# Performance work log

Hardware: AMD Instinct MI355X
Metric: run time of the kernel (lower is better)

## Reference

```python
import jax, jax.numpy as jnp
import numpy as np

B, H, N, M = 8192, 512, 1024, 128
EPS_COS = 1e-8   # torch cosine_similarity default eps
EPS_NORM = 1e-16 # normalization eps in forward


def _linear_params(key, fan_in, fan_out):
    # torch nn.Linear default init: U(-1/sqrt(fan_in), 1/sqrt(fan_in))
    lim = 1.0 / np.sqrt(fan_in)
    kw, kb = jax.random.split(key)
    W = jax.random.uniform(kw, (fan_out, fan_in), minval=-lim, maxval=lim, dtype=jnp.float32)
    b = jax.random.uniform(kb, (fan_out,), minval=-lim, maxval=lim, dtype=jnp.float32)
    return W, b


def setup_inputs() -> dict:
    key = jax.random.key(0)
    ks = jax.random.split(key, 8)
    Wk, bk = _linear_params(ks[0], H, M)
    Wb, bb = _linear_params(ks[1], H, 1)
    Wg, bg = _linear_params(ks[2], H, 1)
    Ws, bs = _linear_params(ks[3], H, N)
    Wgam, bgam = _linear_params(ks[4], H, 1)
    x = jax.random.normal(ks[5], (B, H), dtype=jnp.float32)
    # previous_state is an attention-weight vector over memory rows (sums to 1)
    previous_state = jax.nn.softmax(jax.random.normal(ks[6], (B, N), dtype=jnp.float32), axis=-1)
    memory = jax.random.normal(ks[7], (N, M), dtype=jnp.float32)
    return dict(x=x, previous_state=previous_state, memory=memory,
                Wk=Wk, bk=bk, Wb=Wb, bb=bb, Wg=Wg, bg=bg,
                Ws=Ws, bs=bs, Wgam=Wgam, bgam=bgam)


def _circular_convolution(w, s):
    # Full circular convolution over the memory axis:
    #   out[b, i] = sum_j w[b, j] * s[b, (i - j) mod N]
    # Implemented via FFT to avoid materializing a [B, N, N] shift matrix.
    out = jnp.fft.irfft(jnp.fft.rfft(w, axis=-1) * jnp.fft.rfft(s, axis=-1),
                        n=w.shape[-1], axis=-1)
    # conv of nonnegative weights is nonnegative; clamp tiny FFT round-off
    # negatives so the fractional power below stays well defined.
    return jnp.maximum(out, 0.0)


def reference(x, previous_state, memory, Wk, bk, Wb, bb, Wg, bg, Ws, bs, Wgam, bgam):
    k = x @ Wk.T + bk                                   # [B, M]
    beta = jax.nn.softplus(x @ Wb.T + bb)               # [B, 1]
    g = jax.nn.sigmoid(x @ Wg.T + bg)                   # [B, 1]
    s = jax.nn.softmax(x @ Ws.T + bs, axis=-1)          # [B, N]
    gamma = 1.0 + jax.nn.softplus(x @ Wgam.T + bgam)    # [B, 1]

    # cosine similarity between each key and each memory row -> [B, N]
    k_n = k / jnp.maximum(jnp.linalg.norm(k, axis=-1, keepdims=True), EPS_COS)
    m_n = memory / jnp.maximum(jnp.linalg.norm(memory, axis=-1, keepdims=True), EPS_COS)
    cos = k_n @ m_n.T                                   # [B, N]

    w_c = jax.nn.softmax(beta * cos, axis=1)            # content addressing
    w_g = g * w_c + (1.0 - g) * previous_state          # interpolation gate
    w_t = _circular_convolution(w_g, s)                 # location shift
    w = w_t ** gamma                                    # sharpening
    w = w / (jnp.sum(w, axis=1, keepdims=True) + EPS_NORM)

    read = w @ memory                                   # [B, M]
    return read, w
```

## Files before the change

kernel.cpp:

```cpp
#include <hip/hip_runtime.h>
#include <hip/hip_bf16.h>
#include <hip/hip_fp16.h>

typedef __attribute__((ext_vector_type(8))) short short8;
typedef __attribute__((ext_vector_type(4))) short short4v;
typedef __attribute__((ext_vector_type(4))) float f32x4;

#define B_ROWS 8192
#define HDIM 512
#define NDIM 1024
#define MDIM 128

__device__ __forceinline__ float softplusf(float z) {
  return fmaxf(z, 0.f) + log1pf(__expf(-fabsf(z)));
}
__device__ __forceinline__ unsigned short f2bfu(float f) {
  __hip_bfloat16 h = __float2bfloat16(f);
  return *reinterpret_cast<unsigned short*>(&h);
}
__device__ __forceinline__ short8 pack8(float4 a, float4 b) {
  short8 r;
  r[0] = (short)f2bfu(a.x); r[1] = (short)f2bfu(a.y);
  r[2] = (short)f2bfu(a.z); r[3] = (short)f2bfu(a.w);
  r[4] = (short)f2bfu(b.x); r[5] = (short)f2bfu(b.y);
  r[6] = (short)f2bfu(b.z); r[7] = (short)f2bfu(b.w);
  return r;
}
__device__ __forceinline__ int pad(int i) { return i + (i >> 4); }

__global__ __launch_bounds__(256) void prep_all(
    const float* __restrict__ x, const float* __restrict__ Ws,
    const float* __restrict__ Wk, const float* __restrict__ mem,
    const float* __restrict__ Wb, const float* __restrict__ bb,
    const float* __restrict__ Wg, const float* __restrict__ bg,
    const float* __restrict__ Wgam, const float* __restrict__ bgam,
    short* __restrict__ xb, short* __restrict__ wsb, short* __restrict__ wkb,
    short* __restrict__ mn_bf, short* __restrict__ memT_bf,
    float* __restrict__ bgg)
{
  const int blk = blockIdx.x, t = threadIdx.x;
  if (blk < 512) {
    __shared__ float sredp[4];
    const int half = t >> 7, tl = t & 127;
    const int n = blk * 2 + half;
    const int wid = t >> 6;
    const float v = mem[n * MDIM + tl];
    float ss = v * v;
#pragma unroll
    for (int o = 32; o; o >>= 1) ss += __shfl_xor(ss, o);
    if ((t & 63) == 0) sredp[wid] = ss;
    __syncthreads();
    const float inv = 1.f / fmaxf(sqrtf(sredp[half * 2] + sredp[half * 2 + 1]), 1e-8f);
    mn_bf[n * MDIM + tl] = (short)f2bfu(v * inv);
    memT_bf[(size_t)tl * NDIM + n] = (short)f2bfu(v);
  } else if (blk < 2560) {
    const int wid = t >> 6, lane = t & 63;
    const int b = (blk - 512) * 4 + wid;
    const size_t xo = (size_t)b * HDIM + lane * 8;
    const float4 x0 = *(const float4*)(x + xo);
    const float4 x1 = *(const float4*)(x + xo + 4);
    *(short8*)(xb + xo) = pack8(x0, x1);
    const float4 b0 = *(const float4*)(Wb + lane * 8);
    const float4 b1 = *(const float4*)(Wb + lane * 8 + 4);
    const float4 g0 = *(const float4*)(Wg + lane * 8);
    const float4 g1 = *(const float4*)(Wg + lane * 8 + 4);
    const float4 m0 = *(const float4*)(Wgam + lane * 8);
    const float4 m1 = *(const float4*)(Wgam + lane * 8 + 4);
    float zb = x0.x*b0.x + x0.y*b0.y + x0.z*b0.z + x0.w*b0.w
             + x1.x*b1.x + x1.y*b1.y + x1.z*b1.z + x1.w*b1.w;
    float zg = x0.x*g0.x + x0.y*g0.y + x0.z*g0.z + x0.w*g0.w
             + x1.x*g1.x + x1.y*g1.y + x1.z*g1.z + x1.w*g1.w;
    float zm = x0.x*m0.x + x0.y*m0.y + x0.z*m0.z + x0.w*m0.w
             + x1.x*m1.x + x1.y*m1.y + x1.z*m1.z + x1.w*m1.w;
#pragma unroll
    for (int o = 32; o; o >>= 1) {
      zb += __shfl_xor(zb, o); zg += __shfl_xor(zg, o); zm += __shfl_xor(zm, o);
    }
    if (lane == 0) {
      zb += bb[0]; zg += bg[0]; zm += bgam[0];
      bgg[b * 4 + 0] = softplusf(zb);
      bgg[b * 4 + 1] = 1.f / (1.f + __expf(-zg));
      bgg[b * 4 + 2] = 1.f + softplusf(zm);
    }
  } else {
    const int NS4 = NDIM * HDIM / 4;
    const int NK4 = MDIM * HDIM / 4;
    const int stride = 144 * 256;
    for (int i = (blk - 2560) * 256 + t; i < NS4 + NK4; i += stride) {
      const float* src; short* dst; int j = i;
      if (j < NS4) { src = Ws; dst = wsb; }
      else { j -= NS4; src = Wk; dst = wkb; }
      const float4 v = ((const float4*)src)[j];
      short4v o;
      o[0] = (short)f2bfu(v.x); o[1] = (short)f2bfu(v.y);
      o[2] = (short)f2bfu(v.z); o[3] = (short)f2bfu(v.w);
      ((short4v*)dst)[j] = o;
    }
  }
}

__global__ __launch_bounds__(256) void kgemm_norm(
    const short* __restrict__ xb, const short* __restrict__ wkb,
    const float* __restrict__ bk, short* __restrict__ khat)
{
  __shared__ __align__(16) short sA[32][40];
  __shared__ __align__(16) short sW[128][40];
  __shared__ float snorm[4][32];
  __shared__ float sinv[32];

  const int tid = threadIdx.x, lane = tid & 63, wid = tid >> 6;
  const int bm = blockIdx.x;
  const int fr = lane & 15, kg = (lane >> 4) << 3;

  f32x4 acc[2][2] = {};

  for (int k0 = 0; k0 < HDIM; k0 += 32) {
    if (k0) __syncthreads();
    if (tid < 128) {
      const int row = tid >> 2, c0 = (tid & 3) * 8;
      *(short8*)(&sA[row][c0]) =
          *(const short8*)(xb + (size_t)(bm * 32 + row) * HDIM + k0 + c0);
    }
#pragma unroll
    for (int u = tid; u < 512; u += 256) {
      const int row = u >> 2, c0 = (u & 3) * 8;
      *(short8*)(&sW[row][c0]) =
          *(const short8*)(wkb + (size_t)row * HDIM + k0 + c0);
    }
    __syncthreads();

    short8 af[2], bf[2];
#pragma unroll
    for (int i = 0; i < 2; i++) af[i] = *(const short8*)(&sA[i * 16 + fr][kg]);
#pragma unroll
    for (int n = 0; n < 2; n++) bf[n] = *(const short8*)(&sW[wid * 32 + n * 16 + fr][kg]);
#pragma unroll
    for (int i = 0; i < 2; i++)
#pragma unroll
      for (int n = 0; n < 2; n++)
        acc[i][n] = __builtin_amdgcn_mfma_f32_16x16x32_bf16(af[i], bf[n], acc[i][n], 0, 0, 0);
  }

  const int rbase = (lane >> 4) << 2;
  float z[2][2][4];
#pragma unroll
  for (int i = 0; i < 2; i++)
#pragma unroll
    for (int n = 0; n < 2; n++) {
      const float bv = bk[wid * 32 + n * 16 + fr];
#pragma unroll
      for (int r = 0; r < 4; r++) z[i][n][r] = acc[i][n][r] + bv;
    }
#pragma unroll
  for (int i = 0; i < 2; i++)
#pragma unroll
    for (int r = 0; r < 4; r++) {
      float sq = z[i][0][r] * z[i][0][r] + z[i][1][r] * z[i][1][r];
      sq += __shfl_xor(sq, 1); sq += __shfl_xor(sq, 2);
      sq += __shfl_xor(sq, 4); sq += __shfl_xor(sq, 8);
      if (fr == 0) snorm[wid][i * 16 + rbase + r] = sq;
    }
  __syncthreads();
  if (tid < 32) {
    const float nn = snorm[0][tid] + snorm[1][tid] + snorm[2][tid] + snorm[3][tid];
    sinv[tid] = 1.f / fmaxf(sqrtf(nn), 1e-8f);
  }
  __syncthreads();
#pragma unroll
  for (int i = 0; i < 2; i++)
#pragma unroll
    for (int n = 0; n < 2; n++)
#pragma unroll
      for (int r = 0; r < 4; r++) {
        const int grl = i * 16 + rbase + r;
        khat[(size_t)(bm * 32 + grl) * MDIM + wid * 32 + n * 16 + fr] =
            (short)f2bfu(z[i][n][r] * sinv[grl]);
      }
}

template<int OUTMODE>
__global__ __launch_bounds__(256) void kgemm128(
    const short* __restrict__ A, const short* __restrict__ W,
    const float* __restrict__ bias, void* __restrict__ C,
    int ncols, int K)
{
  __shared__ __align__(16) short sA[128 * 32];
  __shared__ __align__(16) short sB[128 * 32];

  const int tid = threadIdx.x, lane = tid & 63, wid = tid >> 6;
  const int bm = blockIdx.y, bn = blockIdx.x;
  const int wr = wid >> 1, wc = wid & 1;
  const int fr = lane & 15, kg = (lane >> 4) << 3;

  f32x4 acc[4][4] = {};

  for (int k0 = 0; k0 < K; k0 += 32) {
    if (k0) __syncthreads();
#pragma unroll
    for (int j = 0; j < 2; j++) {
      const int c = tid + j * 256;
      const short* g = A + (size_t)(bm * 128 + (c >> 2)) * K + k0 + (c & 3) * 8;
      short* l = &sA[(j * 256 + wid * 64) * 8];
      __builtin_amdgcn_global_load_lds(
          (const __attribute__((address_space(1))) void*)g,
          (__attribute__((address_space(3))) void*)l, 16, 0, 0);
    }
#pragma unroll
    for (int j = 0; j < 2; j++) {
      const int c = tid + j * 256;
      const short* g = W + (size_t)(bn * 128 + (c >> 2)) * K + k0 + (c & 3) * 8;
      short* l = &sB[(j * 256 + wid * 64) * 8];
      __builtin_amdgcn_global_load_lds(
          (const __attribute__((address_space(1))) void*)g,
          (__attribute__((address_space(3))) void*)l, 16, 0, 0);
    }
    __syncthreads();

    short8 af[4], bf[4];
#pragma unroll
    for (int m = 0; m < 4; m++)
      af[m] = *(const short8*)(&sA[(wr * 64 + m * 16 + fr) * 32 + kg]);
#pragma unroll
    for (int n = 0; n < 4; n++)
      bf[n] = *(const short8*)(&sB[(wc * 64 + n * 16 + fr) * 32 + kg]);

#pragma unroll
    for (int m = 0; m < 4; m++)
#pragma unroll
      for (int n = 0; n < 4; n++)
        acc[m][n] = __builtin_amdgcn_mfma_f32_16x16x32_bf16(af[m], bf[n], acc[m][n], 0, 0, 0);
  }

#pragma unroll
  for (int m = 0; m < 4; m++)
#pragma unroll
    for (int n = 0; n < 4; n++) {
      const int gr = bm * 128 + wr * 64 + m * 16 + ((lane >> 4) << 2);
      const int gc = bn * 128 + wc * 64 + n * 16 + fr;
      const float bv = bias ? bias[gc] : 0.f;
#pragma unroll
      for (int r = 0; r < 4; r++) {
        const float v = acc[m][n][r] + bv;
        const size_t idx = (size_t)(gr + r) * ncols + gc;
        if constexpr (OUTMODE == 0) ((float*)C)[idx] = v;
        else ((__half*)C)[idx] = __float2half(v);
      }
    }
}

#define ANG0 (-0.0061359231515425650f)

template<int ST>
__device__ __forceinline__ void fft_mid(const float* __restrict__ sr,
                                        const float* __restrict__ si,
                                        float* __restrict__ dr,
                                        float* __restrict__ di, int tid,
                                        int j0, int j1, int j2, int j3)
{
  const int ls = 2 * ST, s = 1 << ls;
  const int p = tid >> ls, q = tid & (s - 1), tb = tid & ~(s - 1);
  const float a0r = sr[j0], a0i = si[j0], a1r = sr[j1], a1i = si[j1];
  const float a2r = sr[j2], a2i = si[j2], a3r = sr[j3], a3i = si[j3];
  const float b0r = a0r + a2r, b0i = a0i + a2i, b1r = a1r + a3r, b1i = a1i + a3i;
  const float b2r = a0r - a2r, b2i = a0i - a2i, b3r = a1r - a3r, b3i = a1i - a3i;
  const float A0r = b0r + b1r, A0i = b0i + b1i;
  const float A1r = b2r + b3i, A1i = b2i - b3r;
  const float A2r = b0r - b1r, A2i = b0i - b1i;
  const float A3r = b2r - b3i, A3i = b2i + b3r;
  const int o = q + 4 * s * p;
  dr[pad(o)] = A0r; di[pad(o)] = A0i;
  if constexpr (ST < 4) {
    float s1, c1; __sincosf(ANG0 * (float)tb, &s1, &c1);
    const float c2 = c1 * c1 - s1 * s1, s2 = 2.f * s1 * c1;
    const float c3 = c1 * c2 - s1 * s2, s3 = s1 * c2 + c1 * s2;
    dr[pad(o + s)]     = A1r * c1 - A1i * s1; di[pad(o + s)]     = A1r * s1 + A1i * c1;
    dr[pad(o + 2 * s)] = A2r * c2 - A2i * s2; di[pad(o + 2 * s)] = A2r * s2 + A2i * c2;
    dr[pad(o + 3 * s)] = A3r * c3 - A3i * s3; di[pad(o + 3 * s)] = A3r * s3 + A3i * c3;
  } else {
    dr[pad(o + s)]     = A1r; di[pad(o + s)]     = A1i;
    dr[pad(o + 2 * s)] = A2r; di[pad(o + 2 * s)] = A2i;
    dr[pad(o + 3 * s)] = A3r; di[pad(o + 3 * s)] = A3i;
  }
  __syncthreads();
}

template<int J>
__device__ __forceinline__ void fft512_mid(const float* __restrict__ sr,
                                           const float* __restrict__ si,
                                           float* __restrict__ dr,
                                           float* __restrict__ di, int tid)
{
  if (tid < 128) {
    constexpr int s  = (J == 1) ? 2 : (J == 2) ? 8 : 32;
    constexpr int ns = (J == 1) ? 256 : (J == 2) ? 64 : 16;
    constexpr int ls = (J == 1) ? 1 : (J == 2) ? 3 : 5;
    const int p = tid >> ls, q = tid & (s - 1);
    const float a0r = sr[pad(tid)],       a0i = si[pad(tid)];
    const float a1r = sr[pad(tid + 128)], a1i = si[pad(tid + 128)];
    const float a2r = sr[pad(tid + 256)], a2i = si[pad(tid + 256)];
    const float a3r = sr[pad(tid + 384)], a3i = si[pad(tid + 384)];
    const float b0r = a0r + a2r, b0i = a0i + a2i, b1r = a1r + a3r, b1i = a1i + a3i;
    const float b2r = a0r - a2r, b2i = a0i - a2i, b3r = a1r - a3r, b3i = a1i - a3i;
    const float A0r = b0r + b1r, A0i = b0i + b1i;
    const float A1r = b2r + b3i, A1i = b2i - b3r;
    const float A2r = b0r - b1r, A2i = b0i - b1i;
    const float A3r = b2r - b3i, A3i = b2i + b3r;
    float s1, c1; __sincosf((-6.283185307179586f / (float)ns) * (float)p, &s1, &c1);
    const float c2 = c1 * c1 - s1 * s1, s2 = 2.f * s1 * c1;
    const float c3 = c1 * c2 - s1 * s2, s3 = s1 * c2 + c1 * s2;
    const int o = q + 4 * s * p;
    dr[pad(o)]         = A0r;                 di[pad(o)]         = A0i;
    dr[pad(o + s)]     = A1r * c1 - A1i * s1; di[pad(o + s)]     = A1r * s1 + A1i * c1;
    dr[pad(o + 2 * s)] = A2r * c2 - A2i * s2; di[pad(o + 2 * s)] = A2r * s2 + A2i * c2;
    dr[pad(o + 3 * s)] = A3r * c3 - A3i * s3; di[pad(o + 3 * s)] = A3r * s3 + A3i * c3;
  }
  __syncthreads();
}

__global__ __launch_bounds__(256) void rowpass(
    const __half* __restrict__ slogH, const __half* __restrict__ cosbH,
    const float* __restrict__ bgg, const float* __restrict__ prev,
    float* __restrict__ wout, short* __restrict__ wbf)
{
  __shared__ float bAr[1088], bAi[1088], bBr[1088], bBi[1088];
  __shared__ float sred[8];
  const int b = blockIdx.x, tid = threadIdx.x;
  const int lane = tid & 63, wid = tid >> 6;
  const int j0 = pad(tid), j1 = pad(tid + 256), j2 = pad(tid + 512), j3 = pad(tid + 768);

  const float beta = bgg[b * 4 + 0], g = bgg[b * 4 + 1], gamma = bgg[b * 4 + 2];

  float sv[4], cv[4];
  float e1 = 0.f, e2 = 0.f;
#pragma unroll
  for (int i = 0; i < 4; i++) {
    sv[i] = __expf(__half2float(slogH[(size_t)b * NDIM + tid + i * 256]));
    cv[i] = __expf(beta * __half2float(cosbH[(size_t)b * NDIM + tid + i * 256]));
    e1 += sv[i]; e2 += cv[i];
  }
#pragma unroll
  for (int o = 32; o; o >>= 1) { e1 += __shfl_xor(e1, o); e2 += __shfl_xor(e2, o); }
  if (lane == 0) { sred[wid * 2] = e1; sred[wid * 2 + 1] = e2; }
  __syncthreads();
  const float r1 = 1.f / (sred[0] + sred[2] + sred[4] + sred[6]);
  const float r2 = 1.f / (sred[1] + sred[3] + sred[5] + sred[7]);

  float s1, c1; __sincosf(ANG0 * (float)tid, &s1, &c1);
  const float c2 = c1 * c1 - s1 * s1, s2 = 2.f * s1 * c1;
  const float c3 = c1 * c2 - s1 * s2, s3 = s1 * c2 + c1 * s2;

  {
    float ar[4], ai[4];
#pragma unroll
    for (int i = 0; i < 4; i++) {
      const int idx = tid + i * 256;
      const float pv = prev[(size_t)b * NDIM + idx];
      ar[i] = g * cv[i] * r2 + (1.f - g) * pv;
      ai[i] = sv[i] * r1;
    }
    const float b0r = ar[0] + ar[2], b0i = ai[0] + ai[2];
    const float b1r = ar[1] + ar[3], b1i = ai[1] + ai[3];
    const float b2r = ar[0] - ar[2], b2i = ai[0] - ai[2];
    const float b3r = ar[1] - ar[3], b3i = ai[1] - ai[3];
    const float A0r = b0r + b1r, A0i = b0i + b1i;
    const float A1r = b2r + b3i, A1i = b2i - b3r;
    const float A2r = b0r - b1r, A2i = b0i - b1i;
    const float A3r = b2r - b3i, A3i = b2i + b3r;
    const int o4 = 4 * tid;
    bBr[pad(o4)]     = A0r;                  bBi[pad(o4)]     = A0i;
    bBr[pad(o4 + 1)] = A1r * c1 - A1i * s1;  bBi[pad(o4 + 1)] = A1r * s1 + A1i * c1;
    bBr[pad(o4 + 2)] = A2r * c2 - A2i * s2;  bBi[pad(o4 + 2)] = A2r * s2 + A2i * c2;
    bBr[pad(o4 + 3)] = A3r * c3 - A3i * s3;  bBi[pad(o4 + 3)] = A3r * s3 + A3i * c3;
  }
  __syncthreads();

  fft_mid<1>(bBr, bBi, bAr, bAi, tid, j0, j1, j2, j3);
  fft_mid<2>(bAr, bAi, bBr, bBi, tid, j0, j1, j2, j3);
  fft_mid<3>(bBr, bBi, bAr, bAi, tid, j0, j1, j2, j3);
  fft_mid<4>(bAr, bAi, bBr, bBi, tid, j0, j1, j2, j3);

#pragma unroll
  for (int i = 0; i < 2; i++) {
    const int k = tid + i * 256;
    const int kp = pad(k), rp = pad((1024 - k) & 1023);
    const float Zkr = bBr[kp], Zki = bBi[kp];
    const float Zrr = bBr[rp], Zri = bBi[rp];
    const float Wr = 0.5f * (Zkr + Zrr), Wi = 0.5f * (Zki - Zri);
    const float Sr = 0.5f * (Zki + Zri), Si = 0.5f * (Zrr - Zkr);
    bAr[kp] = Wr * Sr - Wi * Si;
    bAi[kp] = Wr * Si + Wi * Sr;
  }
  if (tid == 0) {
    const int kp = pad(512);
    bAr[kp] = bBr[kp] * bBi[kp];
    bAi[kp] = 0.f;
  }
  __syncthreads();

  {
    float es, ec; __sincosf(0.0061359231515425650f * (float)tid, &es, &ec);
    const float P0r = bAr[pad(tid)],        P0i = bAi[pad(tid)];
    const float Pa0r = bAr[pad(512 - tid)], Pa0i = bAi[pad(512 - tid)];
    const float S0r = P0r + Pa0r, S0i = P0i - Pa0i;
    const float D0r = P0r - Pa0r, D0i = P0i + Pa0i;
    const float Q0r = S0r - es * D0r - ec * D0i;
    const float Q0i = S0i + ec * D0r - es * D0i;
    const float P1r = bAr[pad(tid + 256)],  P1i = bAi[pad(tid + 256)];
    const float Pa1r = bAr[pad(256 - tid)], Pa1i = bAi[pad(256 - tid)];
    const float S1r = P1r + Pa1r, S1i = P1i - Pa1i;
    const float D1r = P1r - Pa1r, D1i = P1i + Pa1i;
    const float Q1r = S1r - ec * D1r + es * D1i;
    const float Q1i = S1i - es * D1r - ec * D1i;
    const float ur = Q0r, ui = -Q0i, vr = Q1r, vi = -Q1i;
    float ts, tc; __sincosf(-0.012271846303085130f * (float)tid, &ts, &tc);
    const float d_r = ur - vr, d_i = ui - vi;
    bBr[pad(2 * tid)]     = ur + vr;             bBi[pad(2 * tid)]     = ui + vi;
    bBr[pad(2 * tid + 1)] = d_r * tc - d_i * ts; bBi[pad(2 * tid + 1)] = d_r * ts + d_i * tc;
  }
  __syncthreads();

  fft512_mid<1>(bBr, bBi, bAr, bAi, tid);
  fft512_mid<2>(bAr, bAi, bBr, bBi, tid);
  fft512_mid<3>(bBr, bBi, bAr, bAi, tid);

  if (tid < 128) {
    const int i0 = pad(tid), i1 = pad(tid + 128), i2 = pad(tid + 256), i3 = pad(tid + 384);
    const float a0r = bAr[i0], a0i = bAi[i0], a1r = bAr[i1], a1i = bAi[i1];
    const float a2r = bAr[i2], a2i = bAi[i2], a3r = bAr[i3], a3i = bAi[i3];
    const float b0r = a0r + a2r, b0i = a0i + a2i, b1r = a1r + a3r, b1i = a1i + a3i;
    const float b2r = a0r - a2r, b2i = a0i - a2i, b3r = a1r - a3r, b3i = a1i - a3i;
    bBr[i0] = b0r + b1r; bBi[i0] = b0i + b1i;
    bBr[i1] = b2r + b3i; bBi[i1] = b2i - b3r;
    bBr[i2] = b0r - b1r; bBi[i2] = b0i - b1i;
    bBr[i3] = b2r - b3i; bBi[i3] = b2i + b3r;
  }
  __syncthreads();

  const int m0 = pad(2 * tid), m1 = pad(2 * tid + 1);
  float xv[4];
  xv[0] =  bBr[m0] * (1.f / 1024.f);
  xv[1] = -bBi[m0] * (1.f / 1024.f);
  xv[2] =  bBr[m1] * (1.f / 1024.f);
  xv[3] = -bBi[m1] * (1.f / 1024.f);

  float wt[4]; float esum = 0.f;
#pragma unroll
  for (int i = 0; i < 4; i++) {
    const float v = fmaxf(xv[i], 0.f);
    const float p = (v > 0.f) ? __expf(gamma * __logf(v)) : 0.f;
    wt[i] = p; esum += p;
  }
#pragma unroll
  for (int o = 32; o; o >>= 1) esum += __shfl_xor(esum, o);
  if (lane == 0) sred[wid] = esum;
  __syncthreads();
  const float rn = 1.f / (sred[0] + sred[1] + sred[2] + sred[3] + 1e-16f);
  const float w0 = wt[0] * rn, w1 = wt[1] * rn, w2 = wt[2] * rn, w3 = wt[3] * rn;
  *(float4*)(wout + (size_t)b * NDIM + 4 * tid) = make_float4(w0, w1, w2, w3);
  short4v wb;
  wb[0] = (short)f2bfu(w0); wb[1] = (short)f2bfu(w1);
  wb[2] = (short)f2bfu(w2); wb[3] = (short)f2bfu(w3);
  *(short4v*)(wbf + (size_t)b * NDIM + 4 * tid) = wb;
}

extern "C" void kernel_launch(void* const* d_in, const int* in_sizes, int n_in,
                              void* d_out, int out_size, void* d_ws, size_t ws_size,
                              hipStream_t stream)
{
  const float* x    = (const float*)d_in[0];
  const float* prev = (const float*)d_in[1];
  const float* mem  = (const float*)d_in[2];
  const float* Wk   = (const float*)d_in[3];
  const float* bk   = (const float*)d_in[4];
  const float* Wb   = (const float*)d_in[5];
  const float* bb   = (const float*)d_in[6];
  const float* Wg   = (const float*)d_in[7];
  const float* bg   = (const float*)d_in[8];
  const float* Ws   = (const float*)d_in[9];
  const float* bs   = (const float*)d_in[10];
  const float* Wgam = (const float*)d_in[11];
  const float* bgam = (const float*)d_in[12];

  char* ws = (char*)d_ws;
  short*  mn_bf   = (short*) (ws + 0);
  short*  memT_bf = (short*) (ws + 262144);
  short*  khat    = (short*) (ws + 524288);
  float*  bgg     = (float*) (ws + 2621440);
  __half* slogH   = (__half*)(ws + 2752512);
  __half* cosbH   = (__half*)(ws + 19529728);
  short*  xb      = (short*) (ws + 36306944);
  short*  wsb     = (short*) (ws + 44695552);
  short*  wkb     = (short*) (ws + 45744128);
  short*  wbf     = (short*) (ws + 45875200);

  float* readout = (float*)d_out;
  float* wout = readout + (size_t)B_ROWS * MDIM;

  prep_all<<<2704, 256, 0, stream>>>(x, Ws, Wk, mem, Wb, bb, Wg, bg, Wgam, bgam,
                                     xb, wsb, wkb, mn_bf, memT_bf, bgg);
  kgemm_norm<<<B_ROWS / 32, 256, 0, stream>>>(xb, wkb, bk, khat);
  kgemm128<1><<<dim3(NDIM / 128, B_ROWS / 128), 256, 0, stream>>>(
      xb, wsb, bs, slogH, NDIM, HDIM);
  kgemm128<1><<<dim3(NDIM / 128, B_ROWS / 128), 256, 0, stream>>>(
      khat, mn_bf, nullptr, cosbH, NDIM, MDIM);
  rowpass<<<B_ROWS, 256, 0, stream>>>(slogH, cosbH, bgg, prev, wout, wbf);
  kgemm128<0><<<dim3(1, B_ROWS / 128), 256, 0, stream>>>(
      wbf, memT_bf, nullptr, readout, MDIM, NDIM);
}
```

Measured before the change: 123.7 us.

## Fuse key projection with cosine GEMM and split-K the readout GEMM

Merges the key GEMM plus normalization with the cosine-similarity GEMM in one kernel. The normalized key tile stays in LDS and is multiplied against all 1024 memory rows in chunks of 128, which drops the khat global round trip and one launch. The final readout GEMM, which had only 64 blocks, is split four ways along K into partial buffers and summed by a new reduce kernel, raising parallelism at the cost of extra partial writes and one more launch. The fused kernel uses much more LDS per block (about 45KB), which may lower occupancy.

Result: faster. 117.9 us (-4.7%).

```diff
diff --git a/kernel.cpp b/kernel.cpp
--- a/kernel.cpp
+++ b/kernel.cpp
@@ -99,21 +99,24 @@
   }
 }
 
-__global__ __launch_bounds__(256) void kgemm_norm(
+__global__ __launch_bounds__(256) void kgemm_cos(
     const short* __restrict__ xb, const short* __restrict__ wkb,
-    const float* __restrict__ bk, short* __restrict__ khat)
+    const float* __restrict__ bk, const short* __restrict__ mn_bf,
+    __half* __restrict__ cosbH)
 {
   __shared__ __align__(16) short sA[32][40];
   __shared__ __align__(16) short sW[128][40];
+  __shared__ __align__(16) short skhat[32][136];
+  __shared__ __align__(16) short sMN[128][136];
   __shared__ float snorm[4][32];
   __shared__ float sinv[32];
 
   const int tid = threadIdx.x, lane = tid & 63, wid = tid >> 6;
   const int bm = blockIdx.x;
   const int fr = lane & 15, kg = (lane >> 4) << 3;
+  const int rbase = (lane >> 4) << 2;
 
   f32x4 acc[2][2] = {};
-
   for (int k0 = 0; k0 < HDIM; k0 += 32) {
     if (k0) __syncthreads();
     if (tid < 128) {
@@ -141,7 +144,6 @@
         acc[i][n] = __builtin_amdgcn_mfma_f32_16x16x32_bf16(af[i], bf[n], acc[i][n], 0, 0, 0);
   }
 
-  const int rbase = (lane >> 4) << 2;
   float z[2][2][4];
 #pragma unroll
   for (int i = 0; i < 2; i++)
@@ -172,17 +174,56 @@
     for (int n = 0; n < 2; n++)
 #pragma unroll
       for (int r = 0; r < 4; r++) {
-        const int grl = i * 16 + rbase + r;
-        khat[(size_t)(bm * 32 + grl) * MDIM + wid * 32 + n * 16 + fr] =
-            (short)f2bfu(z[i][n][r] * sinv[grl]);
+        const int row = i * 16 + rbase + r;
+        skhat[row][wid * 32 + n * 16 + fr] = (short)f2bfu(z[i][n][r] * sinv[row]);
       }
+
+  for (int cc = 0; cc < 8; cc++) {
+#pragma unroll
+    for (int i = 0; i < 8; i++) {
+      const int u = tid + i * 256;
+      const int r = u >> 4, c0 = (u & 15) * 8;
+      *(short8*)(&sMN[r][c0]) =
+          *(const short8*)(mn_bf + (size_t)(cc * 128 + r) * MDIM + c0);
+    }
+    __syncthreads();
+
+    f32x4 acc2[2][2] = {};
+#pragma unroll
+    for (int k0 = 0; k0 < 128; k0 += 32) {
+      short8 af2[2], bf2[2];
+#pragma unroll
+      for (int i = 0; i < 2; i++)
+        af2[i] = *(const short8*)(&skhat[i * 16 + fr][k0 + kg]);
+#pragma unroll
+      for (int n = 0; n < 2; n++)
+        bf2[n] = *(const short8*)(&sMN[wid * 32 + n * 16 + fr][k0 + kg]);
+#pragma unroll
+      for (int i = 0; i < 2; i++)
+#pragma unroll
+        for (int n = 0; n < 2; n++)
+          acc2[i][n] = __builtin_amdgcn_mfma_f32_16x16x32_bf16(af2[i], bf2[n], acc2[i][n], 0, 0, 0);
+    }
+    __syncthreads();
+
+#pragma unroll
+    for (int i = 0; i < 2; i++)
+#pragma unroll
+      for (int n = 0; n < 2; n++)
+#pragma unroll
+        for (int r = 0; r < 4; r++) {
+          const int row = i * 16 + rbase + r;
+          const int gc = cc * 128 + wid * 32 + n * 16 + fr;
+          cosbH[(size_t)(bm * 32 + row) * NDIM + gc] = __float2half(acc2[i][n][r]);
+        }
+  }
 }
 
 template<int OUTMODE>
 __global__ __launch_bounds__(256) void kgemm128(
     const short* __restrict__ A, const short* __restrict__ W,
     const float* __restrict__ bias, void* __restrict__ C,
-    int ncols, int K)
+    int ncols, int Kld, int ksplit, size_t cstride)
 {
   __shared__ __align__(16) short sA[128 * 32];
   __shared__ __align__(16) short sB[128 * 32];
@@ -191,15 +232,16 @@
   const int bm = blockIdx.y, bn = blockIdx.x;
   const int wr = wid >> 1, wc = wid & 1;
   const int fr = lane & 15, kg = (lane >> 4) << 3;
+  const int kbeg = blockIdx.z * ksplit, kend = kbeg + ksplit;
 
   f32x4 acc[4][4] = {};
 
-  for (int k0 = 0; k0 < K; k0 += 32) {
-    if (k0) __syncthreads();
+  for (int k0 = kbeg; k0 < kend; k0 += 32) {
+    if (k0 != kbeg) __syncthreads();
 #pragma unroll
     for (int j = 0; j < 2; j++) {
       const int c = tid + j * 256;
-      const short* g = A + (size_t)(bm * 128 + (c >> 2)) * K + k0 + (c & 3) * 8;
+      const short* g = A + (size_t)(bm * 128 + (c >> 2)) * Kld + k0 + (c & 3) * 8;
       short* l = &sA[(j * 256 + wid * 64) * 8];
       __builtin_amdgcn_global_load_lds(
           (const __attribute__((address_space(1))) void*)g,
@@ -208,7 +250,7 @@
 #pragma unroll
     for (int j = 0; j < 2; j++) {
       const int c = tid + j * 256;
-      const short* g = W + (size_t)(bn * 128 + (c >> 2)) * K + k0 + (c & 3) * 8;
+      const short* g = W + (size_t)(bn * 128 + (c >> 2)) * Kld + k0 + (c & 3) * 8;
       short* l = &sB[(j * 256 + wid * 64) * 8];
       __builtin_amdgcn_global_load_lds(
           (const __attribute__((address_space(1))) void*)g,
@@ -241,11 +283,21 @@
 #pragma unroll
       for (int r = 0; r < 4; r++) {
         const float v = acc[m][n][r] + bv;
-        const size_t idx = (size_t)(gr + r) * ncols + gc;
+        const size_t idx = (size_t)(gr + r) * ncols + gc + blockIdx.z * cstride;
         if constexpr (OUTMODE == 0) ((float*)C)[idx] = v;
         else ((__half*)C)[idx] = __float2half(v);
       }
     }
+}
+
+__global__ __launch_bounds__(256) void reduce4(const float* __restrict__ p,
+                                               float* __restrict__ out)
+{
+  const int i = blockIdx.x * 256 + threadIdx.x;
+  const float4* p4 = (const float4*)p;
+  const float4 a = p4[i], b = p4[i + 262144], c = p4[i + 524288], d = p4[i + 786432];
+  ((float4*)out)[i] = make_float4(a.x + b.x + c.x + d.x, a.y + b.y + c.y + d.y,
+                                  a.z + b.z + c.z + d.z, a.w + b.w + c.w + d.w);
 }
 
 #define ANG0 (-0.0061359231515425650f)
@@ -484,26 +536,25 @@
   char* ws = (char*)d_ws;
   short*  mn_bf   = (short*) (ws + 0);
   short*  memT_bf = (short*) (ws + 262144);
-  short*  khat    = (short*) (ws + 524288);
-  float*  bgg     = (float*) (ws + 2621440);
-  __half* slogH   = (__half*)(ws + 2752512);
-  __half* cosbH   = (__half*)(ws + 19529728);
-  short*  xb      = (short*) (ws + 36306944);
-  short*  wsb     = (short*) (ws + 44695552);
-  short*  wkb     = (short*) (ws + 45744128);
-  short*  wbf     = (short*) (ws + 45875200);
+  float*  bgg     = (float*) (ws + 524288);
+  __half* slogH   = (__half*)(ws + 655360);
+  __half* cosbH   = (__half*)(ws + 17432576);
+  short*  xb      = (short*) (ws + 34209792);
+  short*  wsb     = (short*) (ws + 42598400);
+  short*  wkb     = (short*) (ws + 43646976);
+  short*  wbf     = (short*) (ws + 43778048);
+  float*  rpart   = (float*) (ws + 60555264);
 
   float* readout = (float*)d_out;
   float* wout = readout + (size_t)B_ROWS * MDIM;
 
   prep_all<<<2704, 256, 0, stream>>>(x, Ws, Wk, mem, Wb, bb, Wg, bg, Wgam, bgam,
                                      xb, wsb, wkb, mn_bf, memT_bf, bgg);
-  kgemm_norm<<<B_ROWS / 32, 256, 0, stream>>>(xb, wkb, bk, khat);
-  kgemm128<1><<<dim3(NDIM / 128, B_ROWS / 128), 256, 0, stream>>>(
-      xb, wsb, bs, slogH, NDIM, HDIM);
-  kgemm128<1><<<dim3(NDIM / 128, B_ROWS / 128), 256, 0, stream>>>(
-      khat, mn_bf, nullptr, cosbH, NDIM, MDIM);
+  kgemm_cos<<<B_ROWS / 32, 256, 0, stream>>>(xb, wkb, bk, mn_bf, cosbH);
+  kgemm128<1><<<dim3(NDIM / 128, B_ROWS / 128, 1), 256, 0, stream>>>(
+      xb, wsb, bs, slogH, NDIM, HDIM, HDIM, 0);
   rowpass<<<B_ROWS, 256, 0, stream>>>(slogH, cosbH, bgg, prev, wout, wbf);
-  kgemm128<0><<<dim3(1, B_ROWS / 128), 256, 0, stream>>>(
-      wbf, memT_bf, nullptr, readout, MDIM, NDIM);
-}
+  kgemm128<0><<<dim3(1, B_ROWS / 128, 4), 256, 0, stream>>>(
+      wbf, memT_bf, nullptr, rpart, MDIM, NDIM, 256, (size_t)B_ROWS * MDIM);
+  reduce4<<<1024, 256, 0, stream>>>(rpart, readout);
+}
```
